# Optimization experiments

Measured on AMD Instinct MI355X. Metric: run time of the kernel, lower is better.

## Reference

```python
import jax, jax.numpy as jnp
import numpy as np

DIM = 256      # channel dim
NW = 7         # n_win per side
HEADS = 8
TOPK = 4
KVW = 4        # kv_per_win (ada_avgpool output side)
EPS = 1e-6


def _dwconv(x, w, b):
    # depthwise conv, NHWC, 'SAME' == padding k//2 for odd kernels
    y = jax.lax.conv_general_dilated(
        x, w, (1, 1), 'SAME',
        dimension_numbers=('NHWC', 'HWIO', 'NHWC'),
        feature_group_count=x.shape[-1])
    return y + b


def _ln(x, g, b):
    mu = x.mean(-1, keepdims=True)
    var = ((x - mu) ** 2).mean(-1, keepdims=True)
    return (x - mu) * jax.lax.rsqrt(var + EPS) * g + b


def _bra(x, qkv_w, qkv_b, wo_w, wo_b, lepe_w, lepe_b):
    # BiLevelRoutingAttention, x: (n, H, W, C)
    n, H, W, C = x.shape
    hw, ww = H // NW, W // NW          # window size (8, 8)
    scale = C ** -0.5                   # qk_dim ** -0.5 (BiFormer uses full qk_dim)
    qkv = x @ qkv_w.T + qkv_b           # (n, H, W, 3C)
    # window partition: n (j hw) (i ww) c -> n (j i) hw ww c
    qkv_win = qkv.reshape(n, NW, hw, NW, ww, 3 * C)
    qkv_win = qkv_win.transpose(0, 1, 3, 2, 4, 5).reshape(n, NW * NW, hw, ww, 3 * C)
    q = qkv_win[..., :C]                # (n, p2, hw, ww, C)
    kv = qkv_win[..., C:]               # (n, p2, hw, ww, 2C)
    # --- window-level routing (q/k detached in torch; no fwd effect) ---
    q_win = q.mean((2, 3))              # (n, p2, C)
    k_win = kv[..., :C].mean((2, 3))    # (n, p2, C)
    logits = jnp.einsum('npc,nqc->npq', q_win * scale, k_win)
    _, idx = jax.lax.top_k(logits, TOPK)            # (n, p2, k)
    # --- kv downsample: adaptive avg pool (hw,ww)->(KVW,KVW), exact 2x2 mean here ---
    fh, fw = hw // KVW, ww // KVW
    kv_pix = kv.reshape(n, NW * NW, KVW, fh, KVW, fw, 2 * C).mean((3, 5))
    kv_pix = kv_pix.reshape(n, NW * NW, KVW * KVW, 2 * C)   # (n, p2, w2, 2C)
    # --- gather top-k windows' kv ---
    kv_sel = jax.vmap(lambda t, ix: t[ix])(kv_pix, idx)     # (n, p2, k, w2, 2C)
    cph = C // HEADS
    k_sel = kv_sel[..., :C].reshape(n, NW * NW, TOPK * KVW * KVW, HEADS, cph)
    v_sel = kv_sel[..., C:].reshape(n, NW * NW, TOPK * KVW * KVW, HEADS, cph)
    q_pix = q.reshape(n, NW * NW, hw * ww, HEADS, cph)
    # --- windowed attention over gathered tokens ---
    att = jnp.einsum('npqmc,npsmc->npmqs', q_pix * scale, k_sel)
    att = jax.nn.softmax(att, axis=-1)
    out = jnp.einsum('npmqs,npsmc->npqmc', att, v_sel)
    out = out.reshape(n, NW, NW, hw, ww, C).transpose(0, 1, 3, 2, 4, 5).reshape(n, H, W, C)
    # --- lepe: depthwise 5x5 on v over the full image ---
    v_img = qkv[..., 2 * C:]
    out = out + _dwconv(v_img, lepe_w, lepe_b)
    return out @ wo_w.T + wo_b


def setup_inputs() -> dict:
    key = jax.random.key(0)
    ks = jax.random.split(key, 8)
    C, s = DIM, 0.02
    p = {}
    p['x'] = jax.random.normal(ks[0], (16, C, 56, 56), jnp.float32)
    p['pos_w'] = jax.random.normal(ks[1], (3, 3, 1, C), jnp.float32) * s
    p['pos_b'] = jnp.zeros((C,), jnp.float32)
    p['ln1_g'] = jnp.ones((C,), jnp.float32)
    p['ln1_b'] = jnp.zeros((C,), jnp.float32)
    p['ln2_g'] = jnp.ones((C,), jnp.float32)
    p['ln2_b'] = jnp.zeros((C,), jnp.float32)
    p['qkv_w'] = jax.random.normal(ks[2], (3 * C, C), jnp.float32) * s
    p['qkv_b'] = jnp.zeros((3 * C,), jnp.float32)
    p['wo_w'] = jax.random.normal(ks[3], (C, C), jnp.float32) * s
    p['wo_b'] = jnp.zeros((C,), jnp.float32)
    p['lepe_w'] = jax.random.normal(ks[4], (5, 5, 1, C), jnp.float32) * s
    p['lepe_b'] = jnp.zeros((C,), jnp.float32)
    p['fc1_w'] = jax.random.normal(ks[5], (4 * C, C), jnp.float32) * s
    p['fc1_b'] = jnp.zeros((4 * C,), jnp.float32)
    p['fc2_w'] = jax.random.normal(ks[6], (C, 4 * C), jnp.float32) * s
    p['fc2_b'] = jnp.zeros((C,), jnp.float32)
    return p


def reference(x, pos_w, pos_b, ln1_g, ln1_b, ln2_g, ln2_b, qkv_w, qkv_b,
              wo_w, wo_b, lepe_w, lepe_b, fc1_w, fc1_b, fc2_w, fc2_b):
    xh = x.transpose(0, 2, 3, 1)                       # NCHW -> NHWC
    xh = xh + _dwconv(xh, pos_w, pos_b)                # pos embed (dw 3x3)
    xh = xh + _bra(_ln(xh, ln1_g, ln1_b), qkv_w, qkv_b, wo_w, wo_b, lepe_w, lepe_b)
    h = _ln(xh, ln2_g, ln2_b)
    h = jax.nn.gelu(h @ fc1_w.T + fc1_b, approximate=False)
    xh = xh + (h @ fc2_w.T + fc2_b)
    return xh.transpose(0, 3, 1, 2)                    # NHWC -> NCHW
```

## Files before the change

### kernel.cpp

```cpp
#include <hip/hip_runtime.h>
#include <math.h>

static constexpr int NIMG = 16;
static constexpr int TOK  = NIMG * 56 * 56;
static constexpr size_t TC = (size_t)TOK * 256;
static constexpr int PTOK = 784 * 16;

typedef __bf16 bf16x8 __attribute__((ext_vector_type(8)));
typedef float  f32x4  __attribute__((ext_vector_type(4)));

__device__ inline float bf2f(unsigned short u) {
  unsigned int i = ((unsigned int)u) << 16; float f; __builtin_memcpy(&f, &i, 4); return f;
}
__device__ inline unsigned short f2bf(float f) {
  unsigned int i; __builtin_memcpy(&i, &f, 4);
  unsigned int r = i + 0x7fffu + ((i >> 16) & 1u);
  return (unsigned short)(r >> 16);
}

__global__ __launch_bounds__(256) void nchw2nhwc(const float* __restrict__ x,
                                                 float* __restrict__ y) {
  __shared__ float T[32][37];
  int nh = blockIdx.z;
  int n = nh / 56, h = nh % 56;
  int c0 = blockIdx.y * 32, w0 = blockIdx.x * 32;
  int tid = threadIdx.x;
  int wlim = 56 - w0; if (wlim > 32) wlim = 32;
  {
    int ci = tid >> 3, w = (tid & 7) * 4;
    if (w < wlim) {
      f32x4 v = *(const f32x4*)&x[(((size_t)n * 256 + c0 + ci) * 56 + h) * 56 + w0 + w];
#pragma unroll
      for (int j = 0; j < 4; j++) T[ci][w + j] = v[j];
    }
  }
  __syncthreads();
  {
    int wi = tid >> 3, cq = tid & 7;
    if (wi < wlim) {
      f32x4 o;
#pragma unroll
      for (int k = 0; k < 4; k++) o[k] = T[cq * 4 + k][wi];
      *(f32x4*)&y[(((size_t)n * 56 + h) * 56 + w0 + wi) * 256 + c0 + cq * 4] = o;
    }
  }
}

__global__ __launch_bounds__(256) void nhwc2nchw(const float* __restrict__ y,
                                                 float* __restrict__ o) {
  __shared__ float T[32][37];
  int nh = blockIdx.z;
  int n = nh / 56, h = nh % 56;
  int w0 = blockIdx.x * 32, c0 = blockIdx.y * 32;
  int tid = threadIdx.x;
  int wlim = 56 - w0; if (wlim > 32) wlim = 32;
  {
    int wi = tid >> 3, cq = tid & 7;
    if (wi < wlim) {
      f32x4 v = *(const f32x4*)&y[(((size_t)n * 56 + h) * 56 + w0 + wi) * 256 + c0 + cq * 4];
#pragma unroll
      for (int k = 0; k < 4; k++) T[wi][cq * 4 + k] = v[k];
    }
  }
  __syncthreads();
  {
    int ci = tid >> 3, w = (tid & 7) * 4;
    if (w < wlim) {
      f32x4 ov;
#pragma unroll
      for (int j = 0; j < 4; j++) ov[j] = T[w + j][ci];
      *(f32x4*)&o[(((size_t)n * 256 + c0 + ci) * 56 + h) * 56 + w0 + w] = ov;
    }
  }
}

__global__ __launch_bounds__(256) void posln_kernel(const float* __restrict__ xt,
                                                    const float* __restrict__ w,
                                                    const float* __restrict__ bb,
                                                    const float* __restrict__ g1,
                                                    const float* __restrict__ b1,
                                                    float* __restrict__ xh,
                                                    unsigned short* __restrict__ lnb,
                                                    float* __restrict__ murs) {
  int bid = blockIdx.x;
  int wgid = (bid & 7) * 1568 + (bid >> 3);
  int t = wgid * 4 + (threadIdx.x >> 6);
  int lane = threadIdx.x & 63;
  int c = lane * 4;
  int n = t / 3136, rem = t % 3136, h = rem / 56, ww = rem % 56;
  const float* base = xt + (size_t)n * 3136 * 256 + c;

  f32x4 xx[9]; float msk[9];
#pragma unroll
  for (int k = 0; k < 9; k++) {
    int dh = k / 3 - 1, dw = k % 3 - 1;
    int hh = h + dh, wc = ww + dw;
    msk[k] = ((unsigned)hh < 56u && (unsigned)wc < 56u) ? 1.f : 0.f;
    int hcl = hh < 0 ? 0 : (hh > 55 ? 55 : hh);
    int wcl = wc < 0 ? 0 : (wc > 55 ? 55 : wc);
    xx[k] = *(const f32x4*)&base[(size_t)(hcl * 56 + wcl) * 256];
  }
  f32x4 acc = *(const f32x4*)&bb[c];
#pragma unroll
  for (int k = 0; k < 9; k++) {
    f32x4 wv = *(const f32x4*)&w[k * 256 + c];
    acc += xx[k] * (wv * msk[k]);
  }
  f32x4 v = xx[4] + acc;
  *(f32x4*)&xh[(size_t)t * 256 + c] = v;

  float s = v[0] + v[1] + v[2] + v[3];
#pragma unroll
  for (int m = 1; m < 64; m <<= 1) s += __shfl_xor(s, m);
  float mu = s * (1.f / 256.f);
  f32x4 d = v - mu;
  float ss = d[0] * d[0] + d[1] * d[1] + d[2] * d[2] + d[3] * d[3];
#pragma unroll
  for (int m = 1; m < 64; m <<= 1) ss += __shfl_xor(ss, m);
  float rs = rsqrtf(ss * (1.f / 256.f) + 1e-6f);
  f32x4 gg = *(const f32x4*)&g1[c];
  f32x4 b4 = *(const f32x4*)&b1[c];
  f32x4 y = d * rs * gg + b4;
  unsigned short yb[4];
#pragma unroll
  for (int j = 0; j < 4; j++) yb[j] = f2bf(y[j]);
  __builtin_memcpy(lnb + (size_t)t * 256 + c, yb, 8);
  if (lane == 0) {
    murs[2 * (size_t)t] = mu;
    murs[2 * (size_t)t + 1] = rs;
  }
}

template <bool OUTBF, bool LN2F>
__global__ __launch_bounds__(512, 4) void mgemm2(const unsigned short* __restrict__ A, int lda,
                                                 const unsigned short* __restrict__ B, int ldb,
                                                 const float* __restrict__ bias,
                                                 const float* __restrict__ R,
                                                 void* __restrict__ C_,
                                                 int N, int K, int flags, int gx,
                                                 const float* __restrict__ g2,
                                                 const float* __restrict__ b2,
                                                 unsigned short* __restrict__ ob2) {
  __shared__ __attribute__((aligned(16))) char smraw[49152];
  unsigned short* As = (unsigned short*)smraw;
  unsigned short* Bs = (unsigned short*)(smraw + 16384);
  float* slab = (float*)smraw;
  constexpr int SSTR = 260;

  int tid = threadIdx.x;
  int nwg = gridDim.x, bid = blockIdx.x;
  int q8 = nwg >> 3, r8 = nwg & 7;
  int xcd = bid & 7, pos = bid >> 3;
  int wgid = (xcd < r8 ? xcd * (q8 + 1) : r8 * (q8 + 1) + (xcd - r8) * q8) + pos;
  int m0 = (wgid / gx) * 128;
  int n0 = (wgid % gx) * 256;

  int lane = tid & 63, wid = tid >> 6;
  int wr = (wid >> 2) * 64, wc = (wid & 3) * 64;
  int llo = lane & 15, lhi = lane >> 4;

  f32x4 acc[4][4];
#pragma unroll
  for (int i = 0; i < 4; i++)
#pragma unroll
    for (int j = 0; j < 4; j++) acc[i][j] = (f32x4){0.f, 0.f, 0.f, 0.f};

  for (int k0 = 0; k0 < K; k0 += 64) {
#pragma unroll
    for (int i = 0; i < 2; i++) {
      int qa = tid + 512 * i;
      int row = qa >> 3, col = (qa & 7) ^ (row & 7);
      __builtin_amdgcn_global_load_lds(
          (const __attribute__((address_space(1))) unsigned int*)
              (A + (size_t)(m0 + row) * lda + k0 + col * 8),
          (__attribute__((address_space(3))) unsigned int*)(As + qa * 8), 16, 0, 0);
    }
#pragma unroll
    for (int i = 0; i < 4; i++) {
      int qb = tid + 512 * i;
      int row = qb >> 3, col = (qb & 7) ^ (row & 7);
      __builtin_amdgcn_global_load_lds(
          (const __attribute__((address_space(1))) unsigned int*)
              (B + (size_t)(n0 + row) * ldb + k0 + col * 8),
          (__attribute__((address_space(3))) unsigned int*)(Bs + qb * 8), 16, 0, 0);
    }
    __syncthreads();
#pragma unroll
    for (int ks = 0; ks < 2; ks++) {
      int cchunk = ks * 4 + lhi;
      bf16x8 af[4], bfr[4];
#pragma unroll
      for (int mi = 0; mi < 4; mi++) {
        int r = wr + mi * 16 + llo;
        __builtin_memcpy(&af[mi], As + (size_t)r * 64 + (cchunk ^ (r & 7)) * 8, 16);
      }
#pragma unroll
      for (int nj = 0; nj < 4; nj++) {
        int r = wc + nj * 16 + llo;
        __builtin_memcpy(&bfr[nj], Bs + (size_t)r * 64 + (cchunk ^ (r & 7)) * 8, 16);
      }
#pragma unroll
      for (int mi = 0; mi < 4; mi++)
#pragma unroll
        for (int nj = 0; nj < 4; nj++)
          acc[mi][nj] = __builtin_amdgcn_mfma_f32_16x16x32_bf16(af[mi], bfr[nj],
                                                                acc[mi][nj], 0, 0, 0);
    }
    __syncthreads();
  }

#pragma unroll
  for (int s = 0; s < 4; s++) {
    if (wr == (s >> 1) * 64) {
#pragma unroll
      for (int mi2 = 0; mi2 < 2; mi2++) {
        int mi = (s & 1) * 2 + mi2;
#pragma unroll
        for (int nj = 0; nj < 4; nj++) {
          int col = wc + nj * 16 + llo;
#pragma unroll
          for (int j = 0; j < 4; j++)
            slab[(mi2 * 16 + lhi * 4 + j) * SSTR + col] = acc[mi][nj][j];
        }
      }
    }
    __syncthreads();
    int gmBase = m0 + s * 32;
    if (OUTBF) {
#pragma unroll
      for (int i2 = 0; i2 < 2; i2++) {
        int rr = wid * 4 + i2 * 2 + (lane >> 5);
        int col = (lane & 31) * 8;
        f32x4 v0 = *(f32x4*)&slab[rr * SSTR + col];
        f32x4 v1 = *(f32x4*)&slab[rr * SSTR + col + 4];
        if (!(flags & 8)) {
          v0 += *(const f32x4*)&bias[n0 + col];
          v1 += *(const f32x4*)&bias[n0 + col + 4];
        }
        if (flags & 1) {
#pragma unroll
          for (int j = 0; j < 4; j++) {
            v0[j] = 0.5f * v0[j] * (1.0f + erff(v0[j] * 0.70710678118654752f));
            v1[j] = 0.5f * v1[j] * (1.0f + erff(v1[j] * 0.70710678118654752f));
          }
        }
        unsigned short ob[8];
#pragma unroll
        for (int j = 0; j < 4; j++) { ob[j] = f2bf(v0[j]); ob[4 + j] = f2bf(v1[j]); }
        __builtin_memcpy((unsigned short*)C_ + (size_t)(gmBase + rr) * N + n0 + col, ob, 16);
      }
    } else {
#pragma unroll
      for (int i = 0; i < 4; i++) {
        int rr = wid * 4 + i;
        int gm = gmBase + rr;
        int col = lane * 4;
        f32x4 v = *(f32x4*)&slab[rr * SSTR + col];
        if (!(flags & 8)) v += *(const f32x4*)&bias[n0 + col];
        if (flags & 1) {
#pragma unroll
          for (int j = 0; j < 4; j++)
            v[j] = 0.5f * v[j] * (1.0f + erff(v[j] * 0.70710678118654752f));
        }
        if (flags & 2) v += *(const f32x4*)&R[(size_t)gm * N + n0 + col];
        if (LN2F) {
          float sv = v[0] + v[1] + v[2] + v[3];
          float qv = v[0] * v[0] + v[1] * v[1] + v[2] * v[2] + v[3] * v[3];
#pragma unroll
          for (int d = 1; d < 64; d <<= 1) {
            sv += __shfl_xor(sv, d);
            qv += __shfl_xor(qv, d);
          }
          float mu = sv * (1.f / 256.f);
          float var = qv * (1.f / 256.f) - mu * mu;
          float rs = rsqrtf(var + 1e-6f);
          f32x4 g4 = *(const f32x4*)&g2[col];
          f32x4 b4 = *(const f32x4*)&b2[col];
          f32x4 y = (v - mu) * rs * g4 + b4;
          unsigned short yb[4];
#pragma unroll
          for (int j = 0; j < 4; j++) yb[j] = f2bf(y[j]);
          __builtin_memcpy(ob2 + (size_t)gm * 256 + col, yb, 8);
        }
        *(f32x4*)&((float*)C_)[(size_t)gm * N + n0 + col] = v;
      }
    }
    __syncthreads();
  }
}

__global__ __launch_bounds__(256) void prep_kernel(const float* __restrict__ qkv_w,
                                                   const float* __restrict__ qkv_b,
                                                   const float* __restrict__ wo_w,
                                                   const float* __restrict__ fc1_w,
                                                   const float* __restrict__ fc2_w,
                                                   unsigned short* __restrict__ wqv,
                                                   unsigned short* __restrict__ wkv,
                                                   unsigned short* __restrict__ wwo,
                                                   unsigned short* __restrict__ wfc1,
                                                   unsigned short* __restrict__ wfc2,
                                                   float* __restrict__ bqv) {
  int i = blockIdx.x * 256 + threadIdx.x;
  if (i < 65536) { wqv[i] = f2bf(qkv_w[i]); }
  else if (i < 131072) { int j = i - 65536; wqv[65536 + j] = f2bf(qkv_w[512 * 256 + j]); }
  else if (i < 262144) { int j = i - 131072; wkv[j] = f2bf(qkv_w[256 * 256 + j]); }
  else if (i < 327680) { int j = i - 262144; wwo[j] = f2bf(wo_w[j]); }
  else if (i < 589824) { int j = i - 327680; wfc1[j] = f2bf(fc1_w[j]); }
  else if (i < 851968) { int j = i - 589824; wfc2[j] = f2bf(fc2_w[j]); }
  else if (i < 852480) { int j = i - 851968; bqv[j] = qkv_b[j < 256 ? j : j + 256]; }
}

__global__ __launch_bounds__(256) void pool_kernel(const float* __restrict__ xh,
                                                   const float* __restrict__ murs,
                                                   const float* __restrict__ g1,
                                                   const float* __restrict__ b1,
                                                   unsigned short* __restrict__ plx,
                                                   float* __restrict__ wmx) {
  int np = blockIdx.x * 4 + (threadIdx.x >> 6);
  int lane = threadIdx.x & 63;
  int c = lane * 4;
  int n = np / 49, p = np % 49, wr = p / 7, wcq = p % 7;
  f32x4 g4 = *(const f32x4*)&g1[c];
  f32x4 b4 = *(const f32x4*)&b1[c];
  f32x4 tot = (f32x4){0.f, 0.f, 0.f, 0.f};
  for (int s = 0; s < 16; s++) {
    int i = s >> 2, j = s & 3;
    f32x4 z = (f32x4){0.f, 0.f, 0.f, 0.f};
    for (int di = 0; di < 2; di++)
      for (int dj = 0; dj < 2; dj++) {
        size_t t = ((size_t)n * 56 + wr * 8 + i * 2 + di) * 56 + wcq * 8 + j * 2 + dj;
        float mu = murs[2 * t], rs = murs[2 * t + 1];
        f32x4 v = *(const f32x4*)&xh[t * 256 + c];
        z += (v - mu) * rs;
      }
    z *= 0.25f;
    f32x4 cell = z * g4 + b4;
    unsigned short ab[4];
#pragma unroll
    for (int k = 0; k < 4; k++) ab[k] = f2bf(cell[k]);
    __builtin_memcpy(plx + ((size_t)np * 16 + s) * 256 + c, ab, 8);
    tot += z;
  }
  f32x4 wm = tot * (1.f / 16.f) * g4 + b4;
  *(f32x4*)&wmx[(size_t)np * 256 + c] = wm;
}

__global__ __launch_bounds__(256) void winproj_kernel(const float* __restrict__ wmx,
                                                      const float* __restrict__ qkv_w,
                                                      const float* __restrict__ qkv_b,
                                                      float* __restrict__ qkwin) {
  int np = blockIdx.x, t = threadIdx.x;
  __shared__ float xs[256];
  xs[t] = wmx[(size_t)np * 256 + t];
  __syncthreads();
  for (int rep = 0; rep < 2; rep++) {
    int n = t + rep * 256;
    const float* wrow = qkv_w + (size_t)n * 256;
    float s = qkv_b[n];
    for (int c = 0; c < 256; c++) s += xs[c] * wrow[c];
    qkwin[(size_t)np * 512 + n] = s;
  }
}

__global__ __launch_bounds__(64) void topk_kernel(const float* __restrict__ qkwin,
                                                  int* __restrict__ idx) {
  int np = blockIdx.x;
  int n = np / 49;
  int j = threadIdx.x;
  __shared__ float lg[49];
  if (j < 49) {
    const float* qp = qkwin + (size_t)np * 512;
    const float* kp = qkwin + ((size_t)n * 49 + j) * 512 + 256;
    float s = 0.f;
    for (int c = 0; c < 256; c++) s += qp[c] * kp[c];
    lg[j] = s;
  }
  __syncthreads();
  if (j == 0) {
    unsigned long long used = 0ull;
    for (int t = 0; t < 4; t++) {
      float best = -INFINITY;
      int bi = 0;
      for (int q = 0; q < 49; q++)
        if (!((used >> q) & 1ull) && lg[q] > best) { best = lg[q]; bi = q; }
      idx[np * 4 + t] = bi;
      used |= (1ull << bi);
    }
  }
}

__global__ __launch_bounds__(64) void attn_mfma(const unsigned short* __restrict__ qvb,
                                                const unsigned short* __restrict__ kvp,
                                                const int* __restrict__ idx,
                                                unsigned short* __restrict__ out) {
  __shared__ unsigned short Vt[32 * 72];
  __shared__ unsigned short Pl[64 * 72];
  int bid = blockIdx.x;
  int head = bid & 7, np = bid >> 3;
  int n = np / 49, p = np % 49;
  int h0 = (p / 7) * 8, w0 = (p % 7) * 8;
  int lane = threadIdx.x;
  int lhi = lane >> 4, llo = lane & 15;

  int wi4[4];
#pragma unroll
  for (int t = 0; t < 4; t++) wi4[t] = idx[np * 4 + t];

#pragma unroll
  for (int it = 0; it < 4; it++) {
    int cell = lane >> 2;
    int chunk = lane & 3;
    int s = it * 16 + cell;
    const unsigned short* g = kvp + ((size_t)(n * 49 + wi4[it]) * 16 + cell) * 512
                              + 256 + head * 32 + chunk * 8;
    unsigned short vv[8];
    __builtin_memcpy(vv, g, 16);
#pragma unroll
    for (int j = 0; j < 8; j++) Vt[(chunk * 8 + j) * 72 + s] = vv[j];
  }

  bf16x8 qf[4], kf[4];
#pragma unroll
  for (int mi = 0; mi < 4; mi++) {
    int row = mi * 16 + llo;
    int h = h0 + (row >> 3), w = w0 + (row & 7);
    __builtin_memcpy(&qf[mi],
                     qvb + (((size_t)n * 56 + h) * 56 + w) * 512 + head * 32 + lhi * 8, 16);
  }
#pragma unroll
  for (int nj = 0; nj < 4; nj++) {
    __builtin_memcpy(&kf[nj],
                     kvp + ((size_t)(n * 49 + wi4[nj]) * 16 + llo) * 512 + head * 32 + lhi * 8,
                     16);
  }

  f32x4 acc[4][4];
#pragma unroll
  for (int mi = 0; mi < 4; mi++)
#pragma unroll
    for (int nj = 0; nj < 4; nj++) acc[mi][nj] = (f32x4){0.f, 0.f, 0.f, 0.f};
#pragma unroll
  for (int mi = 0; mi < 4; mi++)
#pragma unroll
    for (int nj = 0; nj < 4; nj++)
      acc[mi][nj] = __builtin_amdgcn_mfma_f32_16x16x32_bf16(qf[mi], kf[nj], acc[mi][nj], 0, 0, 0);

#pragma unroll
  for (int mi = 0; mi < 4; mi++)
#pragma unroll
    for (int nj = 0; nj < 4; nj++) acc[mi][nj] *= 0.0625f;
#pragma unroll
  for (int mi = 0; mi < 4; mi++) {
#pragma unroll
    for (int reg = 0; reg < 4; reg++) {
      float m = fmaxf(fmaxf(acc[mi][0][reg], acc[mi][1][reg]),
                      fmaxf(acc[mi][2][reg], acc[mi][3][reg]));
      m = fmaxf(m, __shfl_xor(m, 1));
      m = fmaxf(m, __shfl_xor(m, 2));
      m = fmaxf(m, __shfl_xor(m, 4));
      m = fmaxf(m, __shfl_xor(m, 8));
      float sum = 0.f;
#pragma unroll
      for (int nj = 0; nj < 4; nj++) {
        float e = __expf(acc[mi][nj][reg] - m);
        acc[mi][nj][reg] = e;
        sum += e;
      }
      sum += __shfl_xor(sum, 1);
      sum += __shfl_xor(sum, 2);
      sum += __shfl_xor(sum, 4);
      sum += __shfl_xor(sum, 8);
      float inv = 1.0f / sum;
#pragma unroll
      for (int nj = 0; nj < 4; nj++) acc[mi][nj][reg] *= inv;
    }
  }

#pragma unroll
  for (int mi = 0; mi < 4; mi++)
#pragma unroll
    for (int nj = 0; nj < 4; nj++)
#pragma unroll
      for (int reg = 0; reg < 4; reg++) {
        int row = mi * 16 + lhi * 4 + reg;
        Pl[row * 72 + nj * 16 + llo] = f2bf(acc[mi][nj][reg]);
      }

  f32x4 o[4][2];
#pragma unroll
  for (int mi = 0; mi < 4; mi++)
#pragma unroll
    for (int nc = 0; nc < 2; nc++) o[mi][nc] = (f32x4){0.f, 0.f, 0.f, 0.f};
#pragma unroll
  for (int ks = 0; ks < 2; ks++) {
    bf16x8 pa[4], vb[2];
#pragma unroll
    for (int mi = 0; mi < 4; mi++)
      __builtin_memcpy(&pa[mi], Pl + (mi * 16 + llo) * 72 + ks * 32 + lhi * 8, 16);
#pragma unroll
    for (int nc = 0; nc < 2; nc++)
      __builtin_memcpy(&vb[nc], Vt + (nc * 16 + llo) * 72 + ks * 32 + lhi * 8, 16);
#pragma unroll
    for (int mi = 0; mi < 4; mi++)
#pragma unroll
      for (int nc = 0; nc < 2; nc++)
        o[mi][nc] = __builtin_amdgcn_mfma_f32_16x16x32_bf16(pa[mi], vb[nc], o[mi][nc], 0, 0, 0);
  }

  __syncthreads();
#pragma unroll
  for (int mi = 0; mi < 4; mi++)
#pragma unroll
    for (int nc = 0; nc < 2; nc++)
#pragma unroll
      for (int reg = 0; reg < 4; reg++) {
        int row = mi * 16 + lhi * 4 + reg;
        Pl[row * 40 + nc * 16 + llo] = f2bf(o[mi][nc][reg]);
      }
  __syncthreads();
#pragma unroll
  for (int it = 0; it < 4; it++) {
    int slot = it * 64 + lane;
    int row = slot >> 2, cp = slot & 3;
    unsigned short ov[8];
    __builtin_memcpy(ov, Pl + row * 40 + cp * 8, 16);
    int h = h0 + (row >> 3), w = w0 + (row & 7);
    __builtin_memcpy(out + (((size_t)n * 56 + h) * 56 + w) * 256 + head * 32 + cp * 8, ov, 16);
  }
}

__global__ __launch_bounds__(256) void lepe_kernel(const unsigned short* __restrict__ qvb,
                                                   const float* __restrict__ w,
                                                   const float* __restrict__ b,
                                                   unsigned short* __restrict__ out) {
  int bid = blockIdx.x;
  int wgid = (bid & 7) * 784 + (bid >> 3);
  int t = wgid * 8 + (threadIdx.x >> 5);
  int cg = threadIdx.x & 31;
  int c = cg * 8;
  int n = t / 3136, rem = t % 3136, h = rem / 56, ww = rem % 56;
  const unsigned short* vbase = qvb + (size_t)n * 3136 * 512 + 256 + c;

  float acc[8];
#pragma unroll
  for (int j = 0; j < 8; j++) acc[j] = b[c + j];
#pragma unroll
  for (int k = 0; k < 25; k++) {
    int dh = k / 5 - 2, dw = k % 5 - 2;
    int hh = h + dh, wc = ww + dw;
    float msk = ((unsigned)hh < 56u && (unsigned)wc < 56u) ? 1.f : 0.f;
    int hcl = hh < 0 ? 0 : (hh > 55 ? 55 : hh);
    int wcl = wc < 0 ? 0 : (wc > 55 ? 55 : wc);
    unsigned short vv[8];
    __builtin_memcpy(vv, vbase + (size_t)(hcl * 56 + wcl) * 512, 16);
    const float* wp = w + k * 256 + c;
#pragma unroll
    for (int j = 0; j < 8; j++) acc[j] += bf2f(vv[j]) * (wp[j] * msk);
  }

  size_t o = (size_t)t * 256 + c;
  unsigned short ov[8];
  __builtin_memcpy(ov, out + o, 16);
#pragma unroll
  for (int j = 0; j < 8; j++) ov[j] = f2bf(bf2f(ov[j]) + acc[j]);
  __builtin_memcpy(out + o, ov, 16);
}

extern "C" void kernel_launch(void* const* d_in, const int* in_sizes, int n_in,
                              void* d_out, int out_size, void* d_ws, size_t ws_size,
                              hipStream_t stream) {
  const float* x      = (const float*)d_in[0];
  const float* pos_w  = (const float*)d_in[1];
  const float* pos_b  = (const float*)d_in[2];
  const float* ln1_g  = (const float*)d_in[3];
  const float* ln1_b  = (const float*)d_in[4];
  const float* ln2_g  = (const float*)d_in[5];
  const float* ln2_b  = (const float*)d_in[6];
  const float* qkv_w  = (const float*)d_in[7];
  const float* qkv_b  = (const float*)d_in[8];
  const float* wo_w   = (const float*)d_in[9];
  const float* wo_b   = (const float*)d_in[10];
  const float* lepe_w = (const float*)d_in[11];
  const float* lepe_b = (const float*)d_in[12];
  const float* fc1_w  = (const float*)d_in[13];
  const float* fc1_b  = (const float*)d_in[14];
  const float* fc2_w  = (const float*)d_in[15];
  const float* fc2_b  = (const float*)d_in[16];

  float*          xt   = (float*)d_out;
  unsigned short* qvb  = (unsigned short*)d_out;
  unsigned short* hbuf = (unsigned short*)d_out;

  float*          r2   = (float*)d_ws;
  float*          wmx  = r2 + TC;
  float*          qkw  = wmx + (size_t)784 * 256;
  float*          bqv  = qkw + (size_t)784 * 512;
  unsigned short* lnb  = (unsigned short*)(bqv + 512);
  unsigned short* aob  = lnb;
  unsigned short* ln2b = lnb;
  unsigned short* plx  = lnb + TC;
  unsigned short* kvp  = plx + (size_t)PTOK * 256;
  unsigned short* wqv  = kvp + (size_t)PTOK * 512;
  unsigned short* wkv  = wqv + (size_t)512 * 256;
  unsigned short* wwo  = wkv + (size_t)512 * 256;
  unsigned short* wfc1 = wwo + (size_t)256 * 256;
  unsigned short* wfc2 = wfc1 + (size_t)1024 * 256;
  int*            idx  = (int*)(wfc2 + (size_t)256 * 1024);
  float*          murs = (float*)(idx + 784 * 4);

  prep_kernel<<<3330, 256, 0, stream>>>(qkv_w, qkv_b, wo_w, fc1_w, fc2_w,
                                        wqv, wkv, wwo, wfc1, wfc2, bqv);
  nchw2nhwc<<<dim3(2, 8, NIMG * 56), 256, 0, stream>>>(x, xt);
  posln_kernel<<<TOK / 4, 256, 0, stream>>>(xt, pos_w, pos_b, ln1_g, ln1_b,
                                            r2, lnb, murs);
  pool_kernel<<<196, 256, 0, stream>>>(r2, murs, ln1_g, ln1_b, plx, wmx);
  mgemm2<true, false><<<784, 512, 0, stream>>>(lnb, 256, wqv, 256, bqv, nullptr,
                                               qvb, 512, 256, 0, 2,
                                               nullptr, nullptr, nullptr);
  mgemm2<true, false><<<196, 512, 0, stream>>>(plx, 256, wkv, 256, qkv_b + 256, nullptr,
                                               kvp, 512, 256, 0, 2,
                                               nullptr, nullptr, nullptr);
  winproj_kernel<<<784, 256, 0, stream>>>(wmx, qkv_w, qkv_b, qkw);
  topk_kernel<<<784, 64, 0, stream>>>(qkw, idx);
  attn_mfma<<<6272, 64, 0, stream>>>(qvb, kvp, idx, aob);
  lepe_kernel<<<TOK / 8, 256, 0, stream>>>(qvb, lepe_w, lepe_b, aob);
  mgemm2<false, true><<<392, 512, 0, stream>>>(aob, 256, wwo, 256, wo_b, r2,
                                               r2, 256, 256, 2, 1,
                                               ln2_g, ln2_b, ln2b);
  mgemm2<true, false><<<784, 512, 0, stream>>>(ln2b, 256, wfc1, 256, fc1_b, nullptr,
                                               hbuf, 512, 256, 1, 2,
                                               nullptr, nullptr, nullptr);
  mgemm2<false, false><<<392, 512, 0, stream>>>(hbuf, 512, wfc2, 1024, fc2_b, r2,
                                                r2, 256, 512, 2, 1,
                                                nullptr, nullptr, nullptr);
  mgemm2<true, false><<<784, 512, 0, stream>>>(ln2b, 256, wfc1 + (size_t)512 * 256, 256,
                                               fc1_b + 512, nullptr,
                                               hbuf, 512, 256, 1, 2,
                                               nullptr, nullptr, nullptr);
  mgemm2<false, false><<<392, 512, 0, stream>>>(hbuf, 512, wfc2 + 512, 1024, fc2_b, r2,
                                                r2, 256, 512, 2 | 8, 1,
                                                nullptr, nullptr, nullptr);
  nhwc2nchw<<<dim3(2, 8, NIMG * 56), 256, 0, stream>>>(r2, (float*)d_out);
}
```

Baseline: 447.3 us.

## Stage LePE neighbourhood in shared memory and fuse MLP halves when workspace allows

The LePE depthwise 5x5 conv now loads a clamped 5x12 pixel patch of V into LDS once per block and reuses it across the 8 pixels in the block. The conv weights are pre-converted to bf16 in the prep kernel. Separately, when the workspace is large enough, the MLP runs as one fc1 GEMM over the full 1024 hidden width and one fc2 GEMM with K=1024, instead of two halves that each read-modify-write the residual. This adds a large hidden buffer and drops the flag 8 that the final fc2 call passed in the old split path. It also slightly lowers the precision of the LePE weights.

```diff
diff --git a/kernel.cpp b/kernel.cpp
--- a/kernel.cpp
+++ b/kernel.cpp
@@ -294,12 +294,14 @@
                                                    const float* __restrict__ wo_w,
                                                    const float* __restrict__ fc1_w,
                                                    const float* __restrict__ fc2_w,
+                                                   const float* __restrict__ lepe_w,
                                                    unsigned short* __restrict__ wqv,
                                                    unsigned short* __restrict__ wkv,
                                                    unsigned short* __restrict__ wwo,
                                                    unsigned short* __restrict__ wfc1,
                                                    unsigned short* __restrict__ wfc2,
-                                                   float* __restrict__ bqv) {
+                                                   float* __restrict__ bqv,
+                                                   unsigned short* __restrict__ wlep) {
   int i = blockIdx.x * 256 + threadIdx.x;
   if (i < 65536) { wqv[i] = f2bf(qkv_w[i]); }
   else if (i < 131072) { int j = i - 65536; wqv[65536 + j] = f2bf(qkv_w[512 * 256 + j]); }
@@ -308,6 +310,7 @@
   else if (i < 589824) { int j = i - 327680; wfc1[j] = f2bf(fc1_w[j]); }
   else if (i < 851968) { int j = i - 589824; wfc2[j] = f2bf(fc2_w[j]); }
   else if (i < 852480) { int j = i - 851968; bqv[j] = qkv_b[j < 256 ? j : j + 256]; }
+  else if (i < 858880) { int j = i - 852480; wlep[j] = f2bf(lepe_w[j]); }
 }
 
 __global__ __launch_bounds__(256) void pool_kernel(const float* __restrict__ xh,
@@ -530,40 +533,62 @@
 }
 
 __global__ __launch_bounds__(256) void lepe_kernel(const unsigned short* __restrict__ qvb,
-                                                   const float* __restrict__ w,
+                                                   const unsigned short* __restrict__ wlep,
                                                    const float* __restrict__ b,
                                                    unsigned short* __restrict__ out) {
+  __shared__ unsigned short Vs[60 * 272];
   int bid = blockIdx.x;
   int wgid = (bid & 7) * 784 + (bid >> 3);
-  int t = wgid * 8 + (threadIdx.x >> 5);
-  int cg = threadIdx.x & 31;
+  int tb = wgid * 8;
+  int n = tb / 3136, rem = tb % 3136;
+  int h0 = rem / 56, w0 = rem % 56;
+  int tid = threadIdx.x;
+
+  const unsigned short* vimg = qvb + (size_t)n * 3136 * 512 + 256;
+  {
+    int chunk = tid & 31;
+    for (int s = tid >> 5; s < 60; s += 8) {
+      int r = s / 12, cc = s % 12;
+      int hh = h0 + r - 2; hh = hh < 0 ? 0 : (hh > 55 ? 55 : hh);
+      int wcg = w0 + cc - 2; wcg = wcg < 0 ? 0 : (wcg > 55 ? 55 : wcg);
+      unsigned short tmp[8];
+      __builtin_memcpy(tmp, vimg + (size_t)(hh * 56 + wcg) * 512 + chunk * 8, 16);
+      __builtin_memcpy(&Vs[s * 272 + chunk * 8], tmp, 16);
+    }
+  }
+  __syncthreads();
+
+  int px = tid >> 5;
+  int cg = tid & 31;
   int c = cg * 8;
-  int n = t / 3136, rem = t % 3136, h = rem / 56, ww = rem % 56;
-  const unsigned short* vbase = qvb + (size_t)n * 3136 * 512 + 256 + c;
+  int wq = w0 + px;
 
   float acc[8];
 #pragma unroll
   for (int j = 0; j < 8; j++) acc[j] = b[c + j];
-#pragma unroll
-  for (int k = 0; k < 25; k++) {
-    int dh = k / 5 - 2, dw = k % 5 - 2;
-    int hh = h + dh, wc = ww + dw;
-    float msk = ((unsigned)hh < 56u && (unsigned)wc < 56u) ? 1.f : 0.f;
-    int hcl = hh < 0 ? 0 : (hh > 55 ? 55 : hh);
-    int wcl = wc < 0 ? 0 : (wc > 55 ? 55 : wc);
-    unsigned short vv[8];
-    __builtin_memcpy(vv, vbase + (size_t)(hcl * 56 + wcl) * 512, 16);
-    const float* wp = w + k * 256 + c;
-#pragma unroll
-    for (int j = 0; j < 8; j++) acc[j] += bf2f(vv[j]) * (wp[j] * msk);
-  }
-
-  size_t o = (size_t)t * 256 + c;
+
+#pragma unroll
+  for (int r = 0; r < 5; r++) {
+    float hok = ((unsigned)(h0 + r - 2) < 56u) ? 1.f : 0.f;
+#pragma unroll
+    for (int dc = 0; dc < 5; dc++) {
+      float m = hok * (((unsigned)(wq + dc - 2) < 56u) ? 1.f : 0.f);
+      int slot = r * 12 + px + dc;
+      unsigned short vv[8], wv[8];
+      __builtin_memcpy(vv, &Vs[slot * 272 + cg * 8], 16);
+      __builtin_memcpy(wv, wlep + (r * 5 + dc) * 256 + c, 16);
+#pragma unroll
+      for (int j = 0; j < 8; j++) acc[j] += bf2f(vv[j]) * (bf2f(wv[j]) * m);
+    }
+  }
+
+  size_t o = (size_t)(tb + px) * 256 + c;
   unsigned short ov[8];
   __builtin_memcpy(ov, out + o, 16);
-#pragma unroll
-  for (int j = 0; j < 8; j++) ov[j] = f2bf(bf2f(ov[j]) + acc[j]);
-  __builtin_memcpy(out + o, ov, 16);
+  unsigned short nv[8];
+#pragma unroll
+  for (int j = 0; j < 8; j++) nv[j] = f2bf(bf2f(ov[j]) + acc[j]);
+  __builtin_memcpy(out + o, nv, 16);
 }
 
 extern "C" void kernel_launch(void* const* d_in, const int* in_sizes, int n_in,
@@ -607,9 +632,14 @@
   unsigned short* wfc2 = wfc1 + (size_t)1024 * 256;
   int*            idx  = (int*)(wfc2 + (size_t)256 * 1024);
   float*          murs = (float*)(idx + 784 * 4);
-
-  prep_kernel<<<3330, 256, 0, stream>>>(qkv_w, qkv_b, wo_w, fc1_w, fc2_w,
-                                        wqv, wkv, wwo, wfc1, wfc2, bqv);
+  unsigned short* wlep = (unsigned short*)(murs + (size_t)TOK * 2);
+  unsigned short* hfull = wlep + 6400;
+
+  size_t base_bytes = (size_t)((char*)hfull - (char*)d_ws);
+  bool fullmlp = ws_size >= base_bytes + (size_t)TOK * 1024 * 2;
+
+  prep_kernel<<<3355, 256, 0, stream>>>(qkv_w, qkv_b, wo_w, fc1_w, fc2_w, lepe_w,
+                                        wqv, wkv, wwo, wfc1, wfc2, bqv, wlep);
   nchw2nhwc<<<dim3(2, 8, NIMG * 56), 256, 0, stream>>>(x, xt);
   posln_kernel<<<TOK / 4, 256, 0, stream>>>(xt, pos_w, pos_b, ln1_g, ln1_b,
                                             r2, lnb, murs);
@@ -623,22 +653,31 @@
   winproj_kernel<<<784, 256, 0, stream>>>(wmx, qkv_w, qkv_b, qkw);
   topk_kernel<<<784, 64, 0, stream>>>(qkw, idx);
   attn_mfma<<<6272, 64, 0, stream>>>(qvb, kvp, idx, aob);
-  lepe_kernel<<<TOK / 8, 256, 0, stream>>>(qvb, lepe_w, lepe_b, aob);
+  lepe_kernel<<<TOK / 8, 256, 0, stream>>>(qvb, wlep, lepe_b, aob);
   mgemm2<false, true><<<392, 512, 0, stream>>>(aob, 256, wwo, 256, wo_b, r2,
                                                r2, 256, 256, 2, 1,
                                                ln2_g, ln2_b, ln2b);
-  mgemm2<true, false><<<784, 512, 0, stream>>>(ln2b, 256, wfc1, 256, fc1_b, nullptr,
-                                               hbuf, 512, 256, 1, 2,
-                                               nullptr, nullptr, nullptr);
-  mgemm2<false, false><<<392, 512, 0, stream>>>(hbuf, 512, wfc2, 1024, fc2_b, r2,
-                                                r2, 256, 512, 2, 1,
-                                                nullptr, nullptr, nullptr);
-  mgemm2<true, false><<<784, 512, 0, stream>>>(ln2b, 256, wfc1 + (size_t)512 * 256, 256,
-                                               fc1_b + 512, nullptr,
-                                               hbuf, 512, 256, 1, 2,
-                                               nullptr, nullptr, nullptr);
-  mgemm2<false, false><<<392, 512, 0, stream>>>(hbuf, 512, wfc2 + 512, 1024, fc2_b, r2,
-                                                r2, 256, 512, 2 | 8, 1,
-                                                nullptr, nullptr, nullptr);
+  if (fullmlp) {
+    mgemm2<true, false><<<1568, 512, 0, stream>>>(ln2b, 256, wfc1, 256, fc1_b, nullptr,
+                                                  hfull, 1024, 256, 1, 4,
+                                                  nullptr, nullptr, nullptr);
+    mgemm2<false, false><<<392, 512, 0, stream>>>(hfull, 1024, wfc2, 1024, fc2_b, r2,
+                                                  r2, 256, 1024, 2, 1,
+                                                  nullptr, nullptr, nullptr);
+  } else {
+    mgemm2<true, false><<<784, 512, 0, stream>>>(ln2b, 256, wfc1, 256, fc1_b, nullptr,
+                                                 hbuf, 512, 256, 1, 2,
+                                                 nullptr, nullptr, nullptr);
+    mgemm2<false, false><<<392, 512, 0, stream>>>(hbuf, 512, wfc2, 1024, fc2_b, r2,
+                                                  r2, 256, 512, 2, 1,
+                                                  nullptr, nullptr, nullptr);
+    mgemm2<true, false><<<784, 512, 0, stream>>>(ln2b, 256, wfc1 + (size_t)512 * 256, 256,
+                                                 fc1_b + 512, nullptr,
+                                                 hbuf, 512, 256, 1, 2,
+                                                 nullptr, nullptr, nullptr);
+    mgemm2<false, false><<<392, 512, 0, stream>>>(hbuf, 512, wfc2 + 512, 1024, fc2_b, r2,
+                                                  r2, 256, 512, 2 | 8, 1,
+                                                  nullptr, nullptr, nullptr);
+  }
   nhwc2nchw<<<dim3(2, 8, NIMG * 56), 256, 0, stream>>>(r2, (float*)d_out);
 }
```

Result: no change. 445.9 us (-0.3%).
